# Kernel optimization log

Hardware: AMD Instinct MI355X
Metric: run time of the kernel (lower is better)

## Reference

```python
import jax, jax.numpy as jnp
import numpy as np
import math

B, R, D = 2048, 512, 256
OUT = 1


def setup_inputs() -> dict:
    key = jax.random.key(0)
    k1, k2, k3, k4 = jax.random.split(key, 4)
    x = jax.random.normal(k1, (B, D), dtype=jnp.float32)
    th = jnp.zeros((R, D), dtype=jnp.float32)
    sign_param = jax.random.normal(k2, (R, D), dtype=jnp.float32) * 0.1
    mask_logit = jnp.full((R, D), -2.0, dtype=jnp.float32)
    log_kappa = jnp.asarray(math.log(6.0), dtype=jnp.float32)
    head_w = jax.random.normal(k3, (OUT, R), dtype=jnp.float32) * (1.0 / np.sqrt(R))
    head_b = jnp.zeros((OUT,), dtype=jnp.float32)
    return {"x": x, "th": th, "sign_param": sign_param,
            "mask_logit": mask_logit, "log_kappa": log_kappa,
            "head_w": head_w, "head_b": head_b}


def _corner_product_z(x, th, sign_param, mask_logit, log_kappa):
    # x: (B, D); th/sign_param/mask_logit: (R, D)
    kappa = jnp.exp(log_kappa)
    sgn = jnp.tanh(sign_param)                 # soft sign in (-1, 1), (R, D)
    # one-sided threshold predicate, broadcast to (B, R, D)
    s = jax.nn.sigmoid(kappa * sgn[None, :, :] * (x[:, None, :] - th[None, :, :]))
    m = jax.nn.sigmoid(mask_logit)             # soft feature mask, (R, D)
    gated = 1.0 - m[None, :, :] * (1.0 - s)    # masked predicate; m->0 => 1 (ignored)
    z = jnp.prod(gated, axis=-1)               # product over features -> (B, R)
    return z, s, m


def reference(x, th, sign_param, mask_logit, log_kappa, head_w, head_b):
    z, _, _ = _corner_product_z(x, th, sign_param, mask_logit, log_kappa)
    y = z @ head_w.T + head_b                  # (B, OUT)
    return y[..., 0] if OUT == 1 else y
```

## Files before the change

kernel.cpp:

```cpp
#include <hip/hip_runtime.h>
#include <math.h>

#define B_TOT 2048
#define R_TOT 512
#define D_TOT 256
#define LOG2E 1.4426950408889634f
#define SCALE_C 2.220446049250313e-16f

typedef float vf4 __attribute__((ext_vector_type(4)));
typedef float vf2 __attribute__((ext_vector_type(2)));


__global__ void prep_kernel(const float* __restrict__ th,
                            const float* __restrict__ sp,
                            const float* __restrict__ ml,
                            const float* __restrict__ lk,
                            float* __restrict__ pp) {
    int idx = blockIdx.x * 256 + threadIdx.x;
    if (idx >= R_TOT * D_TOT) return;
    float kmul = -LOG2E * __builtin_amdgcn_exp2f(lk[0] * LOG2E);
    float u  = sp[idx];
    float eu = __builtin_amdgcn_exp2f(2.0f * LOG2E * u);
    float t  = 1.0f - 2.0f * __builtin_amdgcn_rcpf(eu + 1.0f);
    float A  = kmul * t;
    float Bc = -A * th[idx];
    float em = __builtin_amdgcn_exp2f(LOG2E * ml[idx]);
    float m1 = __builtin_amdgcn_rcpf(1.0f + em);
    int d = idx & 255;
    pp[idx]                       = A;
    pp[R_TOT * D_TOT + idx]       = Bc;
    pp[2 * R_TOT * D_TOT + idx]   = m1 * (((d & 7) == 0) ? SCALE_C : 1.0f);
}

static __device__ __forceinline__ float pair_swap(float v) {
    int i = __builtin_amdgcn_mov_dpp(__float_as_int(v), 0xB1, 0xF, 0xF, true);
    return __int_as_float(i);
}

__global__ __launch_bounds__(256, 4) void main_kernel(
        const float* __restrict__ x,
        const float* __restrict__ pp,
        const float* __restrict__ head_w,
        const float* __restrict__ head_b,
        float*       __restrict__ y) {
    __shared__ float rbuf[4][16][36];
    __shared__ float wz[4][16];

    const int tid  = threadIdx.x;
    const int lane = tid & 63;
    const int wave = tid >> 6;
    const int r0   = (blockIdx.x << 2) + wave;
    const int b0   = blockIdx.y << 4;

    const vf4* pA = (const vf4*)pp                         + r0 * 64 + lane;
    const vf4* pB = (const vf4*)(pp + R_TOT * D_TOT)       + r0 * 64 + lane;
    const vf4* pM = (const vf4*)(pp + 2 * R_TOT * D_TOT)   + r0 * 64 + lane;
    vf4 A  = *pA;
    vf4 Bc = *pB;
    vf4 Ms = *pM;
    const float kx = (lane & 1) ? 1.0f : SCALE_C;
    const vf4 K = {kx, 1.0f, 1.0f, 1.0f};

    const vf4* xv = (const vf4*)x + (size_t)b0 * 64 + lane;

    float r8[16];
    #pragma unroll
    for (int b = 0; b < 16; b++) {
        vf4 xb = xv[b * 64];
        vf4 t  = A * xb + Bc;
        vf4 e;
        e.x = __builtin_amdgcn_exp2f(t.x);
        e.y = __builtin_amdgcn_exp2f(t.y);
        e.z = __builtin_amdgcn_exp2f(t.z);
        e.w = __builtin_amdgcn_exp2f(t.w);
        vf4 n  = Ms * e + K;
        vf4 dd = e * K + K;
        vf2 hn = n.lo * n.hi;
        vf2 hd = dd.lo * dd.hi;
        float np = hn.x * hn.y;
        float dp = hd.x * hd.y;
        float np8 = np * pair_swap(np);
        float dp8 = dp * pair_swap(dp);
        r8[b] = np8 * __builtin_amdgcn_rcpf(dp8);
    }

    if (!(lane & 1)) {
        #pragma unroll
        for (int b = 0; b < 16; b++)
            rbuf[wave][b][lane >> 1] = r8[b];
    }
    __syncthreads();

    if (lane < 16) {
        const float* rb = &rbuf[wave][lane][0];
        vf4 a0 = *(const vf4*)(rb)      * *(const vf4*)(rb + 4);
        vf4 a1 = *(const vf4*)(rb + 8)  * *(const vf4*)(rb + 12);
        vf4 a2 = *(const vf4*)(rb + 16) * *(const vf4*)(rb + 20);
        vf4 a3 = *(const vf4*)(rb + 24) * *(const vf4*)(rb + 28);
        vf4 m  = (a0 * a1) * (a2 * a3);
        vf2 h  = m.lo * m.hi;
        float z = h.x * h.y;
        wz[wave][lane] = head_w[r0] * z;
    }
    __syncthreads();

    if (wave == 0 && lane < 16) {
        float s = wz[0][lane] + wz[1][lane] + wz[2][lane] + wz[3][lane];
        if (blockIdx.x == 0) s += head_b[0];
        atomicAdd(&y[b0 + lane], s);
    }
}

extern "C" void kernel_launch(void* const* d_in, const int* in_sizes, int n_in,
                              void* d_out, int out_size, void* d_ws, size_t ws_size,
                              hipStream_t stream) {
    const float* x  = (const float*)d_in[0];
    const float* th = (const float*)d_in[1];
    const float* sp = (const float*)d_in[2];
    const float* ml = (const float*)d_in[3];
    const float* lk = (const float*)d_in[4];
    const float* hw = (const float*)d_in[5];
    const float* hb = (const float*)d_in[6];
    float* y = (float*)d_out;

    float* pp = (float*)d_ws;

    hipMemsetAsync(y, 0, (size_t)out_size * sizeof(float), stream);
    prep_kernel<<<R_TOT, 256, 0, stream>>>(th, sp, ml, lk, pp);
    dim3 grid(R_TOT / 4, B_TOT / 16, 1);
    main_kernel<<<grid, 256, 0, stream>>>(x, pp, hw, hb, y);
}
```

Measured before the change: 126.1 us.

## Fuse parameter prep into main kernel and loop over eight batch groups per block

Removes the separate prep kernel and its workspace round trip: each wave now computes the tanh/sigmoid-derived coefficients for its row in registers. Each block then loops over eight 16-row batch groups, so that parameter setup and the launch cost are amortized over more work. The grid shrinks accordingly and launch bounds are raised to target more resident blocks. The trade-off is fewer blocks with a longer serial loop and an extra barrier per iteration, plus the coefficients are recomputed once per batch-block instead of once overall.

Result: slower. 291.3 us (+131.1%).

```diff
diff --git a/kernel.cpp b/kernel.cpp
--- a/kernel.cpp
+++ b/kernel.cpp
@@ -11,35 +11,33 @@
 typedef float vf2 __attribute__((ext_vector_type(2)));
 
 
-__global__ void prep_kernel(const float* __restrict__ th,
-                            const float* __restrict__ sp,
-                            const float* __restrict__ ml,
-                            const float* __restrict__ lk,
-                            float* __restrict__ pp) {
-    int idx = blockIdx.x * 256 + threadIdx.x;
-    if (idx >= R_TOT * D_TOT) return;
-    float kmul = -LOG2E * __builtin_amdgcn_exp2f(lk[0] * LOG2E);
-    float u  = sp[idx];
-    float eu = __builtin_amdgcn_exp2f(2.0f * LOG2E * u);
-    float t  = 1.0f - 2.0f * __builtin_amdgcn_rcpf(eu + 1.0f);
-    float A  = kmul * t;
-    float Bc = -A * th[idx];
-    float em = __builtin_amdgcn_exp2f(LOG2E * ml[idx]);
-    float m1 = __builtin_amdgcn_rcpf(1.0f + em);
-    int d = idx & 255;
-    pp[idx]                       = A;
-    pp[R_TOT * D_TOT + idx]       = Bc;
-    pp[2 * R_TOT * D_TOT + idx]   = m1 * (((d & 7) == 0) ? SCALE_C : 1.0f);
-}
-
 static __device__ __forceinline__ float pair_swap(float v) {
     int i = __builtin_amdgcn_mov_dpp(__float_as_int(v), 0xB1, 0xF, 0xF, true);
     return __int_as_float(i);
 }
+static __device__ __forceinline__ vf4 exp2v(vf4 t) {
+    vf4 e;
+    e.x = __builtin_amdgcn_exp2f(t.x);
+    e.y = __builtin_amdgcn_exp2f(t.y);
+    e.z = __builtin_amdgcn_exp2f(t.z);
+    e.w = __builtin_amdgcn_exp2f(t.w);
+    return e;
+}
+static __device__ __forceinline__ vf4 rcpv(vf4 t) {
+    vf4 e;
+    e.x = __builtin_amdgcn_rcpf(t.x);
+    e.y = __builtin_amdgcn_rcpf(t.y);
+    e.z = __builtin_amdgcn_rcpf(t.z);
+    e.w = __builtin_amdgcn_rcpf(t.w);
+    return e;
+}
 
-__global__ __launch_bounds__(256, 4) void main_kernel(
+__global__ __launch_bounds__(256, 8) void main_kernel(
         const float* __restrict__ x,
-        const float* __restrict__ pp,
+        const float* __restrict__ th,
+        const float* __restrict__ sp,
+        const float* __restrict__ ml,
+        const float* __restrict__ lk,
         const float* __restrict__ head_w,
         const float* __restrict__ head_b,
         float*       __restrict__ y) {
@@ -50,64 +48,66 @@
     const int lane = tid & 63;
     const int wave = tid >> 6;
     const int r0   = (blockIdx.x << 2) + wave;
-    const int b0   = blockIdx.y << 4;
+    const int bgg0 = blockIdx.y << 3;
 
-    const vf4* pA = (const vf4*)pp                         + r0 * 64 + lane;
-    const vf4* pB = (const vf4*)(pp + R_TOT * D_TOT)       + r0 * 64 + lane;
-    const vf4* pM = (const vf4*)(pp + 2 * R_TOT * D_TOT)   + r0 * 64 + lane;
-    vf4 A  = *pA;
-    vf4 Bc = *pB;
-    vf4 Ms = *pM;
+    const float kmul = -LOG2E * __builtin_amdgcn_exp2f(lk[0] * LOG2E);
+    const size_t pidx = (size_t)r0 * 64 + lane;
+    const vf4 one = {1.0f, 1.0f, 1.0f, 1.0f};
+    vf4 u   = ((const vf4*)sp)[pidx];
+    vf4 eu  = exp2v((2.0f * LOG2E) * u);
+    vf4 tt  = one - 2.0f * rcpv(eu + one);
+    vf4 A   = kmul * tt;
+    vf4 Bc  = (-A) * ((const vf4*)th)[pidx];
+    vf4 em  = exp2v(LOG2E * ((const vf4*)ml)[pidx]);
+    vf4 Ms  = rcpv(one + em);
     const float kx = (lane & 1) ? 1.0f : SCALE_C;
+    Ms.x *= kx;
     const vf4 K = {kx, 1.0f, 1.0f, 1.0f};
+    const float w_r = head_w[r0];
 
-    const vf4* xv = (const vf4*)x + (size_t)b0 * 64 + lane;
+    for (int g = 0; g < 8; g++) {
+        const int b0 = (bgg0 + g) << 4;
+        const vf4* xv = (const vf4*)x + (size_t)b0 * 64 + lane;
 
-    float r8[16];
-    #pragma unroll
-    for (int b = 0; b < 16; b++) {
-        vf4 xb = xv[b * 64];
-        vf4 t  = A * xb + Bc;
-        vf4 e;
-        e.x = __builtin_amdgcn_exp2f(t.x);
-        e.y = __builtin_amdgcn_exp2f(t.y);
-        e.z = __builtin_amdgcn_exp2f(t.z);
-        e.w = __builtin_amdgcn_exp2f(t.w);
-        vf4 n  = Ms * e + K;
-        vf4 dd = e * K + K;
-        vf2 hn = n.lo * n.hi;
-        vf2 hd = dd.lo * dd.hi;
-        float np = hn.x * hn.y;
-        float dp = hd.x * hd.y;
-        float np8 = np * pair_swap(np);
-        float dp8 = dp * pair_swap(dp);
-        r8[b] = np8 * __builtin_amdgcn_rcpf(dp8);
-    }
+        float r8[16];
+        #pragma unroll
+        for (int b = 0; b < 16; b++) {
+            vf4 xb = xv[b * 64];
+            vf4 t  = A * xb + Bc;
+            vf4 e  = exp2v(t);
+            vf4 n  = Ms * e + K;
+            vf4 dd = e * K + K;
+            vf2 hn = n.lo * n.hi;
+            vf2 hd = dd.lo * dd.hi;
+            float np = hn.x * hn.y;
+            float dp = hd.x * hd.y;
+            float np8 = np * pair_swap(np);
+            float dp8 = dp * pair_swap(dp);
+            r8[b] = np8 * __builtin_amdgcn_rcpf(dp8);
+        }
 
-    if (!(lane & 1)) {
-        #pragma unroll
-        for (int b = 0; b < 16; b++)
-            rbuf[wave][b][lane >> 1] = r8[b];
-    }
-    __syncthreads();
-
-    if (lane < 16) {
-        const float* rb = &rbuf[wave][lane][0];
-        vf4 a0 = *(const vf4*)(rb)      * *(const vf4*)(rb + 4);
-        vf4 a1 = *(const vf4*)(rb + 8)  * *(const vf4*)(rb + 12);
-        vf4 a2 = *(const vf4*)(rb + 16) * *(const vf4*)(rb + 20);
-        vf4 a3 = *(const vf4*)(rb + 24) * *(const vf4*)(rb + 28);
-        vf4 m  = (a0 * a1) * (a2 * a3);
-        vf2 h  = m.lo * m.hi;
-        float z = h.x * h.y;
-        wz[wave][lane] = head_w[r0] * z;
-    }
-    __syncthreads();
-
-    if (wave == 0 && lane < 16) {
-        float s = wz[0][lane] + wz[1][lane] + wz[2][lane] + wz[3][lane];
-        if (blockIdx.x == 0) s += head_b[0];
-        atomicAdd(&y[b0 + lane], s);
+        if (!(lane & 1)) {
+            #pragma unroll
+            for (int b = 0; b < 16; b++)
+                rbuf[wave][b][lane >> 1] = r8[b];
+        }
+        if (lane < 16) {
+            const float* rb = &rbuf[wave][lane][0];
+            vf4 a0 = *(const vf4*)(rb)      * *(const vf4*)(rb + 4);
+            vf4 a1 = *(const vf4*)(rb + 8)  * *(const vf4*)(rb + 12);
+            vf4 a2 = *(const vf4*)(rb + 16) * *(const vf4*)(rb + 20);
+            vf4 a3 = *(const vf4*)(rb + 24) * *(const vf4*)(rb + 28);
+            vf4 m  = (a0 * a1) * (a2 * a3);
+            vf2 h  = m.lo * m.hi;
+            wz[wave][lane] = w_r * (h.x * h.y);
+        }
+        __syncthreads();
+        if (wave == 0 && lane < 16) {
+            float s = wz[0][lane] + wz[1][lane] + wz[2][lane] + wz[3][lane];
+            if (blockIdx.x == 0) s += head_b[0];
+            atomicAdd(&y[b0 + lane], s);
+        }
+        __syncthreads();
     }
 }
 
@@ -123,10 +123,7 @@
     const float* hb = (const float*)d_in[6];
     float* y = (float*)d_out;
 
-    float* pp = (float*)d_ws;
-
     hipMemsetAsync(y, 0, (size_t)out_size * sizeof(float), stream);
-    prep_kernel<<<R_TOT, 256, 0, stream>>>(th, sp, ml, lk, pp);
-    dim3 grid(R_TOT / 4, B_TOT / 16, 1);
-    main_kernel<<<grid, 256, 0, stream>>>(x, pp, hw, hb, y);
+    dim3 grid(R_TOT / 4, B_TOT / 128, 1);
+    main_kernel<<<grid, 256, 0, stream>>>(x, th, sp, ml, lk, hw, hb, y);
 }
```

## Register-block 4 rules per wave and loop over batch groups with prefetch

Applied to the files above, without the earlier changes.

Each wave now keeps parameters for 4 rules in registers and processes 4 batch rows per step, looping over 8 batch groups per block while prefetching the next x rows. The grid shrinks by 8x in the batch dimension, and cross-block reduction moves to per-wave DPP shuffles plus atomics. The per-4-element ratio is now taken before the pair product, which drops the SCALE_C underflow trick. This targets parameter reload traffic and block sync overhead, at the cost of more registers, fewer blocks and more atomics per output.

New measurement: 132.8 us. +5.3%, slower.

```diff
diff --git a/kernel.cpp b/kernel.cpp
--- a/kernel.cpp
+++ b/kernel.cpp
@@ -5,7 +5,7 @@
 #define R_TOT 512
 #define D_TOT 256
 #define LOG2E 1.4426950408889634f
-#define SCALE_C 2.220446049250313e-16f
+#define NPLANE (R_TOT * D_TOT)
 
 typedef float vf4 __attribute__((ext_vector_type(4)));
 typedef float vf2 __attribute__((ext_vector_type(2)));
@@ -17,7 +17,7 @@
                             const float* __restrict__ lk,
                             float* __restrict__ pp) {
     int idx = blockIdx.x * 256 + threadIdx.x;
-    if (idx >= R_TOT * D_TOT) return;
+    if (idx >= NPLANE) return;
     float kmul = -LOG2E * __builtin_amdgcn_exp2f(lk[0] * LOG2E);
     float u  = sp[idx];
     float eu = __builtin_amdgcn_exp2f(2.0f * LOG2E * u);
@@ -26,15 +26,26 @@
     float Bc = -A * th[idx];
     float em = __builtin_amdgcn_exp2f(LOG2E * ml[idx]);
     float m1 = __builtin_amdgcn_rcpf(1.0f + em);
-    int d = idx & 255;
-    pp[idx]                       = A;
-    pp[R_TOT * D_TOT + idx]       = Bc;
-    pp[2 * R_TOT * D_TOT + idx]   = m1 * (((d & 7) == 0) ? SCALE_C : 1.0f);
+    pp[idx]              = A;
+    pp[NPLANE + idx]     = Bc;
+    pp[2 * NPLANE + idx] = m1;
 }
 
-static __device__ __forceinline__ float pair_swap(float v) {
+static __device__ __forceinline__ float dpp_xor1(float v) {
     int i = __builtin_amdgcn_mov_dpp(__float_as_int(v), 0xB1, 0xF, 0xF, true);
     return __int_as_float(i);
+}
+static __device__ __forceinline__ float dpp_xor2(float v) {
+    int i = __builtin_amdgcn_mov_dpp(__float_as_int(v), 0x4E, 0xF, 0xF, true);
+    return __int_as_float(i);
+}
+static __device__ __forceinline__ vf4 exp2v(vf4 t) {
+    vf4 e;
+    e.x = __builtin_amdgcn_exp2f(t.x);
+    e.y = __builtin_amdgcn_exp2f(t.y);
+    e.z = __builtin_amdgcn_exp2f(t.z);
+    e.w = __builtin_amdgcn_exp2f(t.w);
+    return e;
 }
 
 __global__ __launch_bounds__(256, 4) void main_kernel(
@@ -44,70 +55,82 @@
         const float* __restrict__ head_b,
         float*       __restrict__ y) {
     __shared__ float rbuf[4][16][36];
-    __shared__ float wz[4][16];
 
-    const int tid  = threadIdx.x;
-    const int lane = tid & 63;
-    const int wave = tid >> 6;
-    const int r0   = (blockIdx.x << 2) + wave;
-    const int b0   = blockIdx.y << 4;
+    const int tid   = threadIdx.x;
+    const int lane  = tid & 63;
+    const int wave  = tid >> 6;
+    const int rbase = blockIdx.x << 2;
+    const int bgg0  = blockIdx.y << 3;
 
-    const vf4* pA = (const vf4*)pp                         + r0 * 64 + lane;
-    const vf4* pB = (const vf4*)(pp + R_TOT * D_TOT)       + r0 * 64 + lane;
-    const vf4* pM = (const vf4*)(pp + 2 * R_TOT * D_TOT)   + r0 * 64 + lane;
-    vf4 A  = *pA;
-    vf4 Bc = *pB;
-    vf4 Ms = *pM;
-    const float kx = (lane & 1) ? 1.0f : SCALE_C;
-    const vf4 K = {kx, 1.0f, 1.0f, 1.0f};
+    vf4 A[4], Bc[4], Ms[4];
+    #pragma unroll
+    for (int j = 0; j < 4; j++) {
+        size_t pidx = (size_t)(rbase + j) * 64 + lane;
+        A[j]  = ((const vf4*)pp)[pidx];
+        Bc[j] = ((const vf4*)(pp + NPLANE))[pidx];
+        Ms[j] = ((const vf4*)(pp + 2 * NPLANE))[pidx];
+    }
+    const vf4 one = {1.0f, 1.0f, 1.0f, 1.0f};
+    float w0 = head_w[rbase], w1 = head_w[rbase + 1];
+    float w2 = head_w[rbase + 2], w3 = head_w[rbase + 3];
+    int lj = lane & 3;
+    float wsel = (lj == 0) ? w0 : ((lj == 1) ? w1 : ((lj == 2) ? w2 : w3));
+    const float bias = (blockIdx.x == 0) ? head_b[0] : 0.0f;
 
-    const vf4* xv = (const vf4*)x + (size_t)b0 * 64 + lane;
+    const vf4* xbase = (const vf4*)x
+                       + ((size_t)(bgg0 * 16 + (wave << 2))) * 64 + lane;
 
-    float r8[16];
+    vf4 cur[4], nxt[4];
     #pragma unroll
-    for (int b = 0; b < 16; b++) {
-        vf4 xb = xv[b * 64];
-        vf4 t  = A * xb + Bc;
-        vf4 e;
-        e.x = __builtin_amdgcn_exp2f(t.x);
-        e.y = __builtin_amdgcn_exp2f(t.y);
-        e.z = __builtin_amdgcn_exp2f(t.z);
-        e.w = __builtin_amdgcn_exp2f(t.w);
-        vf4 n  = Ms * e + K;
-        vf4 dd = e * K + K;
-        vf2 hn = n.lo * n.hi;
-        vf2 hd = dd.lo * dd.hi;
-        float np = hn.x * hn.y;
-        float dp = hd.x * hd.y;
-        float np8 = np * pair_swap(np);
-        float dp8 = dp * pair_swap(dp);
-        r8[b] = np8 * __builtin_amdgcn_rcpf(dp8);
-    }
+    for (int i = 0; i < 4; i++) cur[i] = xbase[i * 64];
 
-    if (!(lane & 1)) {
+    #pragma unroll 1
+    for (int g = 0; g < 8; g++) {
+        int gn = (g < 7) ? g + 1 : 7;
         #pragma unroll
-        for (int b = 0; b < 16; b++)
-            rbuf[wave][b][lane >> 1] = r8[b];
-    }
-    __syncthreads();
+        for (int i = 0; i < 4; i++) nxt[i] = xbase[gn * 1024 + i * 64];
+        __builtin_amdgcn_sched_barrier(0);
 
-    if (lane < 16) {
-        const float* rb = &rbuf[wave][lane][0];
-        vf4 a0 = *(const vf4*)(rb)      * *(const vf4*)(rb + 4);
-        vf4 a1 = *(const vf4*)(rb + 8)  * *(const vf4*)(rb + 12);
-        vf4 a2 = *(const vf4*)(rb + 16) * *(const vf4*)(rb + 20);
-        vf4 a3 = *(const vf4*)(rb + 24) * *(const vf4*)(rb + 28);
-        vf4 m  = (a0 * a1) * (a2 * a3);
-        vf2 h  = m.lo * m.hi;
-        float z = h.x * h.y;
-        wz[wave][lane] = head_w[r0] * z;
-    }
-    __syncthreads();
+        #pragma unroll
+        for (int i = 0; i < 4; i++) {
+            vf4 xb = cur[i];
+            #pragma unroll
+            for (int j = 0; j < 4; j++) {
+                vf4 t  = A[j] * xb + Bc[j];
+                vf4 e  = exp2v(t);
+                vf4 n  = Ms[j] * e + one;
+                vf4 dd = e + one;
+                vf2 hn = n.lo * n.hi;
+                vf2 hd = dd.lo * dd.hi;
+                float np = hn.x * hn.y;
+                float dp = hd.x * hd.y;
+                float r4 = np * __builtin_amdgcn_rcpf(dp);
+                float r8 = r4 * dpp_xor1(r4);
+                if (!(lane & 1))
+                    rbuf[wave][i * 4 + j][lane >> 1] = r8;
+            }
+        }
 
-    if (wave == 0 && lane < 16) {
-        float s = wz[0][lane] + wz[1][lane] + wz[2][lane] + wz[3][lane];
-        if (blockIdx.x == 0) s += head_b[0];
-        atomicAdd(&y[b0 + lane], s);
+        if (lane < 16) {
+            const float* rb = &rbuf[wave][lane][0];
+            vf4 a0 = *(const vf4*)(rb)      * *(const vf4*)(rb + 4);
+            vf4 a1 = *(const vf4*)(rb + 8)  * *(const vf4*)(rb + 12);
+            vf4 a2 = *(const vf4*)(rb + 16) * *(const vf4*)(rb + 20);
+            vf4 a3 = *(const vf4*)(rb + 24) * *(const vf4*)(rb + 28);
+            vf4 m  = (a0 * a1) * (a2 * a3);
+            vf2 h  = m.lo * m.hi;
+            float z  = h.x * h.y;
+            float t  = wsel * z;
+            float t1 = t + dpp_xor1(t);
+            float t2 = t1 + dpp_xor2(t1);
+            if ((lane & 3) == 0) {
+                int b = ((bgg0 + g) << 4) + (wave << 2) + (lane >> 2);
+                atomicAdd(&y[b], t2 + bias);
+            }
+        }
+
+        #pragma unroll
+        for (int i = 0; i < 4; i++) cur[i] = nxt[i];
     }
 }
 
@@ -126,7 +149,7 @@
     float* pp = (float*)d_ws;
 
     hipMemsetAsync(y, 0, (size_t)out_size * sizeof(float), stream);
-    prep_kernel<<<R_TOT, 256, 0, stream>>>(th, sp, ml, lk, pp);
-    dim3 grid(R_TOT / 4, B_TOT / 16, 1);
+    prep_kernel<<<NPLANE / 256, 256, 0, stream>>>(th, sp, ml, lk, pp);
+    dim3 grid(R_TOT / 4, B_TOT / 128, 1);
     main_kernel<<<grid, 256, 0, stream>>>(x, pp, hw, hb, y);
 }
```
